# Kernel optimization log

Measured on AMD Instinct MI355X. Metric: run time of the kernel, lower is better.

## Reference

```python
import jax, jax.numpy as jnp
import numpy as np
import math

B, N, C = 4, 8192, 384
H = 6
D = C // H  # head_dim = 64


def setup_inputs() -> dict:
    key = jax.random.key(0)
    ks = jax.random.split(key, 9)
    s = 1.0 / math.sqrt(D)
    x = jax.random.normal(ks[0], (B, N, C), dtype=jnp.float32)
    Wq = jax.random.normal(ks[1], (H, D, D), dtype=jnp.float32) * s
    bq = jax.random.normal(ks[2], (H, D), dtype=jnp.float32) * 0.01
    Wk = jax.random.normal(ks[3], (H, D, D), dtype=jnp.float32) * s
    bk = jax.random.normal(ks[4], (H, D), dtype=jnp.float32) * 0.01
    Wv = jax.random.normal(ks[5], (H, D, D), dtype=jnp.float32) * s
    bv = jax.random.normal(ks[6], (H, D), dtype=jnp.float32) * 0.01
    Wp = jax.random.normal(ks[7], (C, C), dtype=jnp.float32) * (1.0 / math.sqrt(C))
    bp = jax.random.normal(ks[8], (C,), dtype=jnp.float32) * 0.01
    return {"x": x, "Wq": Wq, "bq": bq, "Wk": Wk, "bk": bk,
            "Wv": Wv, "bv": bv, "Wp": Wp, "bp": bp}


def reference(x, Wq, bq, Wk, bk, Wv, bv, Wp, bp):
    b, n, c = x.shape
    # [B, H, N, D]
    xh = x.reshape(b, n, H, D).transpose(0, 2, 1, 3)
    # Batched per-head projections (replaces the Python loop of per-head Linears)
    q = jnp.einsum('bhnd,hde->bhne', xh, Wq) + bq[:, None, :]
    k = jnp.einsum('bhnd,hde->bhne', xh, Wk) + bk[:, None, :]
    v = jnp.einsum('bhnd,hde->bhne', xh, Wv) + bv[:, None, :]
    q = jax.nn.softmax(q, axis=-1)          # over feature dim
    k = jax.nn.softmax(k, axis=-2)          # over sequence dim
    v = v * (1.0 / math.sqrt(D))
    kv = jnp.einsum('bhnd,bhne->bhde', k, v)   # [B,H,D,D] context
    out = jnp.einsum('bhnd,bhde->bhne', q, kv) # [B,H,N,D]
    out = out.transpose(0, 2, 1, 3).reshape(b, n, c)
    return out @ Wp.T + bp
```

## Files before the change

### kernel.cpp

```cpp
#include <hip/hip_runtime.h>
#include <hip/hip_bf16.h>


#define B 4
#define N 8192
#define C 384
#define H 6
#define D 64
#define BH (B * H)
#define BN (B * N)

typedef __attribute__((ext_vector_type(8))) short short8;
typedef __attribute__((ext_vector_type(4))) float f32x4;

__device__ inline unsigned short f2bf(float f) {
    unsigned int u = __float_as_uint(f);
    unsigned int r = (u + 0x7fff + ((u >> 16) & 1)) >> 16;
    return (unsigned short)r;
}

__device__ inline unsigned int cvt2bf(float a, float b) {
    unsigned int r;
    asm("v_cvt_pk_bf16_f32 %0, %1, %2" : "=v"(r) : "v"(a), "v"(b));
    return r;
}

__global__ void wprep(const float* __restrict__ Wq, const float* __restrict__ Wk,
                      const float* __restrict__ Wv, unsigned short* __restrict__ Wt,
                      float* __restrict__ kvraw)
{
    __shared__ float tmp[64][65];
    const int m = blockIdx.x / H;
    const int h = blockIdx.x % H;
    const float* in = (m == 0 ? Wq : m == 1 ? Wk : Wv) + h * 64 * 64;
    const int t = threadIdx.x;
    for (int d = 0; d < 64; ++d) tmp[d][t] = in[d * 64 + t];
    __syncthreads();
    const size_t base = ((size_t)(m * H + h)) * 64 * 64;
    for (int e = 0; e < 64; ++e)
        Wt[base + e * 64 + t] = f2bf(tmp[t][e]);

    const int gid = blockIdx.x * 64 + t;
    const float4 z = {0.f, 0.f, 0.f, 0.f};
    for (int i = gid; i < 24960; i += 1152)
        *(float4*)&kvraw[i * 4] = z;
}

__global__ __launch_bounds__(256, 3) void proj_kernel(
    const float* __restrict__ x, const unsigned short* __restrict__ Wt,
    const float* __restrict__ bq, const float* __restrict__ bk,
    const float* __restrict__ bv,
    unsigned short* __restrict__ qout,
    float* __restrict__ kvraw, float* __restrict__ Sg)
{
    __shared__ __align__(16) char smem[34816];
    unsigned short* W_s = (unsigned short*)smem;
    unsigned short* qbuf = (unsigned short*)(smem + 24576);
    float* kvred = (float*)smem;
    float* sred  = (float*)(smem + 33792);

    const int blk = blockIdx.x;
    const int nb  = blk & 31;
    const int bh  = blk >> 5;
    const int b   = bh / H;
    const int h   = bh % H;
    const int n0  = nb * 256;
    const int t   = threadIdx.x;
    const int lane = t & 63;
    const int w   = t >> 6;
    const int lq  = lane & 15;
    const int qd  = lane >> 4;

    {
        const size_t hb = (size_t)h * 4096;
        for (int id = t; id < 512; id += 256) {
            int e = id >> 3, c = id & 7;
            int dc = ((c ^ (e & 7)) * 8);
            #pragma unroll
            for (int m = 0; m < 3; ++m)
                *(uint4*)&W_s[m * 4096 + e * 64 + dc] =
                    *(const uint4*)(Wt + (size_t)m * H * 4096 + hb + e * 64 + c * 8);
        }
    }

    float bqv[4], bkv[4], bvv[4];
    #pragma unroll
    for (int j = 0; j < 4; ++j) {
        int col = j * 16 + lq;
        bqv[j] = bq[h * D + col];
        bkv[j] = bk[h * D + col];
        bvv[j] = bv[h * D + col];
    }

    unsigned short* qw = qbuf + w * 1152;

    __syncthreads();

    f32x4 kvacc[4][4] = {};
    float sacc[4] = {};

    for (int sub = 0; sub < 4; ++sub) {
        const int ns = n0 + sub * 64;

        const float* ap = x + (size_t)(b * N + ns + w * 16 + lq) * C + h * D + qd * 8;
        short8 af[2];
        {
            float av[16];
            *(float4*)&av[0]  = *(const float4*)ap;
            *(float4*)&av[4]  = *(const float4*)(ap + 4);
            *(float4*)&av[8]  = *(const float4*)(ap + 32);
            *(float4*)&av[12] = *(const float4*)(ap + 36);
            unsigned int* afu = (unsigned int*)af;
            #pragma unroll
            for (int p = 0; p < 8; ++p)
                afu[p] = cvt2bf(av[2 * p], av[2 * p + 1]);
        }

        {
            f32x4 acc[4] = {};
            #pragma unroll
            for (int ck = 0; ck < 2; ++ck)
                #pragma unroll
                for (int j = 0; j < 4; ++j) {
                    const int pc = ((ck * 4 + qd) ^ (lq & 7)) * 8;
                    short8 bw = *(const short8*)&W_s[(j * 16 + lq) * 64 + pc];
                    acc[j] = __builtin_amdgcn_mfma_f32_16x16x32_bf16(af[ck], bw, acc[j], 0, 0, 0);
                }
            #pragma unroll
            for (int r = 0; r < 4; ++r) {
                float e0 = __expf(acc[0][r] + bqv[0]);
                float e1 = __expf(acc[1][r] + bqv[1]);
                float e2 = __expf(acc[2][r] + bqv[2]);
                float e3 = __expf(acc[3][r] + bqv[3]);
                float s = (e0 + e1) + (e2 + e3);
                #pragma unroll
                for (int msk = 1; msk < 16; msk <<= 1) s += __shfl_xor(s, msk);
                float inv = __builtin_amdgcn_rcpf(s);
                unsigned int p01 = cvt2bf(e0 * inv, e1 * inv);
                unsigned int p23 = cvt2bf(e2 * inv, e3 * inv);
                const int row = qd * 4 + r;
                qw[row * 72 + 0 * 16 + lq] = (unsigned short)p01;
                qw[row * 72 + 1 * 16 + lq] = (unsigned short)(p01 >> 16);
                qw[row * 72 + 2 * 16 + lq] = (unsigned short)p23;
                qw[row * 72 + 3 * 16 + lq] = (unsigned short)(p23 >> 16);
            }
            const size_t gbase = (size_t)bh * N + ns + w * 16;
            #pragma unroll
            for (int rep = 0; rep < 2; ++rep) {
                int flat = rep * 64 + lane;
                int row = flat >> 3, c8 = flat & 7;
                *(uint4*)&qout[(gbase + row) * 64 + c8 * 8] =
                    *(uint4*)&qw[row * 72 + c8 * 8];
            }
        }
        __builtin_amdgcn_sched_barrier(0);

        short8 kfrag[4];
        {
            f32x4 acc[4] = {};
            #pragma unroll
            for (int ck = 0; ck < 2; ++ck)
                #pragma unroll
                for (int j = 0; j < 4; ++j) {
                    const int pc = ((ck * 4 + qd) ^ (lq & 7)) * 8;
                    short8 bw = *(const short8*)&W_s[4096 + (j * 16 + lq) * 64 + pc];
                    acc[j] = __builtin_amdgcn_mfma_f32_16x16x32_bf16(af[ck], bw, acc[j], 0, 0, 0);
                }
            #pragma unroll
            for (int j = 0; j < 4; ++j) {
                float e0 = __expf(acc[j][0] + bkv[j]);
                float e1 = __expf(acc[j][1] + bkv[j]);
                float e2 = __expf(acc[j][2] + bkv[j]);
                float e3 = __expf(acc[j][3] + bkv[j]);
                float cs = (e0 + e1) + (e2 + e3);
                cs += __shfl_xor(cs, 16);
                cs += __shfl_xor(cs, 32);
                sacc[j] += cs;
                unsigned int* kf = (unsigned int*)&kfrag[j];
                kf[0] = cvt2bf(e0, e1);
                kf[1] = cvt2bf(e2, e3);
                kf[2] = 0;
                kf[3] = 0;
            }
        }
        __builtin_amdgcn_sched_barrier(0);

        {
            f32x4 acc[4] = {};
            #pragma unroll
            for (int ck = 0; ck < 2; ++ck)
                #pragma unroll
                for (int j = 0; j < 4; ++j) {
                    const int pc = ((ck * 4 + qd) ^ (lq & 7)) * 8;
                    short8 bw = *(const short8*)&W_s[2 * 4096 + (j * 16 + lq) * 64 + pc];
                    acc[j] = __builtin_amdgcn_mfma_f32_16x16x32_bf16(af[ck], bw, acc[j], 0, 0, 0);
                }
            short8 vfrag[4];
            #pragma unroll
            for (int j = 0; j < 4; ++j) {
                float v0 = (acc[j][0] + bvv[j]) * 0.125f;
                float v1 = (acc[j][1] + bvv[j]) * 0.125f;
                float v2 = (acc[j][2] + bvv[j]) * 0.125f;
                float v3 = (acc[j][3] + bvv[j]) * 0.125f;
                unsigned int* vf = (unsigned int*)&vfrag[j];
                vf[0] = cvt2bf(v0, v1);
                vf[1] = cvt2bf(v2, v3);
                vf[2] = 0;
                vf[3] = 0;
            }
            #pragma unroll
            for (int i = 0; i < 4; ++i)
                #pragma unroll
                for (int j = 0; j < 4; ++j)
                    kvacc[i][j] = __builtin_amdgcn_mfma_f32_16x16x32_bf16(
                        kfrag[i], vfrag[j], kvacc[i][j], 0, 0, 0);
        }
        __builtin_amdgcn_sched_barrier(0);
    }

    __syncthreads();

    #pragma unroll
    for (int half = 0; half < 2; ++half) {
        #pragma unroll
        for (int i2 = 0; i2 < 2; ++i2) {
            const int ii = half * 2 + i2;
            #pragma unroll
            for (int j = 0; j < 4; ++j)
                #pragma unroll
                for (int r = 0; r < 4; ++r)
                    kvred[w * 2112 + (i2 * 16 + qd * 4 + r) * 66 + j * 16 + lq] =
                        kvacc[ii][j][r];
        }
        if (half == 0 && qd == 0) {
            #pragma unroll
            for (int j = 0; j < 4; ++j) sred[w * 64 + j * 16 + lq] = sacc[j];
        }
        __syncthreads();
        for (int idx = t; idx < 2048; idx += 256) {
            int dl = idx >> 6, e = idx & 63;
            float s = kvred[dl * 66 + e] + kvred[2112 + dl * 66 + e]
                    + kvred[2 * 2112 + dl * 66 + e] + kvred[3 * 2112 + dl * 66 + e];
            atomicAdd(&kvraw[bh * 4096 + (half * 32 + dl) * 64 + e], s);
        }
        if (half == 1 && t < 64) {
            float s = sred[t] + sred[64 + t] + sred[128 + t] + sred[192 + t];
            atomicAdd(&Sg[bh * 64 + t], s);
        }
        if (half == 0) __syncthreads();
    }
}

__global__ __launch_bounds__(256) void kw_kernel(
    const float* __restrict__ kvraw, const float* __restrict__ Sg,
    const float* __restrict__ Wp, unsigned short* __restrict__ KWT)
{
    __shared__ float kv_s[64 * 68];
    __shared__ float w_s[64 * 68];
    __shared__ float rS_s[64];
    const int bh = blockIdx.x / (C / 64);
    const int ct = blockIdx.x % (C / 64);
    const int b = bh / H, h = bh % H;
    const int c0 = ct * 64;
    const int t = threadIdx.x, dg = t >> 4, cg = t & 15;

    if (t < 64) rS_s[t] = 1.f / Sg[bh * 64 + t];
    __syncthreads();

    for (int i = t; i < 4096; i += 256) {
        int row = i >> 6, e = i & 63;
        kv_s[e * 68 + row] = kvraw[bh * (D * D) + row * 64 + e] * rS_s[row];
        w_s[e * 68 + row]  = Wp[(size_t)(c0 + row) * C + h * 64 + e];
    }
    __syncthreads();

    float acc[4][4] = {};
    for (int e = 0; e < 64; ++e) {
        float4 a = *(float4*)&kv_s[e * 68 + dg * 4];
        float4 w = *(float4*)&w_s[e * 68 + cg * 4];
        const float a4[4] = {a.x, a.y, a.z, a.w};
        const float w4[4] = {w.x, w.y, w.z, w.w};
        #pragma unroll
        for (int i = 0; i < 4; ++i)
            #pragma unroll
            for (int j = 0; j < 4; ++j) acc[i][j] += a4[i] * w4[j];
    }
    #pragma unroll
    for (int i = 0; i < 4; ++i)
        #pragma unroll
        for (int j = 0; j < 4; ++j) {
            int d = dg * 4 + i, c = c0 + cg * 4 + j;
            KWT[((size_t)b * C + c) * (H * D) + h * 64 + d] = f2bf(acc[i][j]);
        }
}

__global__ __launch_bounds__(256) void out_gemm(
    const unsigned short* __restrict__ q, const unsigned short* __restrict__ KWT,
    const float* __restrict__ bp, float* __restrict__ out)
{
    __shared__ __align__(16) unsigned short A_s[128 * 72];
    __shared__ __align__(16) unsigned short B_s[128 * 72];

    const int bid = blockIdx.x;
    const int grp = bid / 24;
    const int rem = bid % 24;
    const int ct  = rem >> 3;
    const int mt  = grp * 8 + (rem & 7);
    const int m0 = mt * 128, c0 = ct * 128;
    const int b  = m0 >> 13;
    const int n0 = m0 & (N - 1);
    const int t  = threadIdx.x;
    const int lane = t & 63;
    const int w  = t >> 6;
    const int wm = w >> 1, wn = w & 1;
    const int lq = lane & 15;
    const int qd = lane >> 4;

    f32x4 acc[4][4] = {};

    for (int h = 0; h < H; ++h) {
        if (h) __syncthreads();
        const unsigned short* qb = q + (size_t)(b * H + h) * N * D + (size_t)n0 * D;
        const unsigned short* kb = KWT + ((size_t)b * C + c0) * (H * D) + h * 64;
        #pragma unroll
        for (int it = 0; it < 4; ++it) {
            int id = it * 256 + t;
            int r = id >> 3, c8 = id & 7;
            *(uint4*)&A_s[r * 72 + c8 * 8] = *(const uint4*)(qb + r * 64 + c8 * 8);
            *(uint4*)&B_s[r * 72 + c8 * 8] = *(const uint4*)(kb + (size_t)r * (H * D) + c8 * 8);
        }
        __syncthreads();

        #pragma unroll
        for (int kk = 0; kk < 64; kk += 32) {
            short8 af[4], bf[4];
            #pragma unroll
            for (int i = 0; i < 4; ++i)
                af[i] = *(short8*)&A_s[(wm * 64 + i * 16 + lq) * 72 + kk + qd * 8];
            #pragma unroll
            for (int j = 0; j < 4; ++j)
                bf[j] = *(short8*)&B_s[(wn * 64 + j * 16 + lq) * 72 + kk + qd * 8];
            #pragma unroll
            for (int i = 0; i < 4; ++i)
                #pragma unroll
                for (int j = 0; j < 4; ++j)
                    acc[i][j] = __builtin_amdgcn_mfma_f32_16x16x32_bf16(
                        af[i], bf[j], acc[i][j], 0, 0, 0);
        }
    }

    float bpv[4];
    #pragma unroll
    for (int j = 0; j < 4; ++j) bpv[j] = bp[c0 + wn * 64 + j * 16 + lq];

    #pragma unroll
    for (int i = 0; i < 4; ++i) {
        #pragma unroll
        for (int r = 0; r < 4; ++r) {
            size_t row = (size_t)m0 + wm * 64 + i * 16 + qd * 4 + r;
            float* orow = out + row * C + c0 + wn * 64;
            #pragma unroll
            for (int j = 0; j < 4; ++j)
                orow[j * 16 + lq] = acc[i][j][r] + bpv[j];
        }
    }
}

extern "C" void kernel_launch(void* const* d_in, const int* in_sizes, int n_in,
                              void* d_out, int out_size, void* d_ws, size_t ws_size,
                              hipStream_t stream)
{
    const float* x  = (const float*)d_in[0];
    const float* Wq = (const float*)d_in[1];
    const float* bq = (const float*)d_in[2];
    const float* Wk = (const float*)d_in[3];
    const float* bk = (const float*)d_in[4];
    const float* Wv = (const float*)d_in[5];
    const float* bv = (const float*)d_in[6];
    const float* Wp = (const float*)d_in[7];
    const float* bp = (const float*)d_in[8];
    float* out = (float*)d_out;

    const size_t SZ = (size_t)B * H * N * D;
    float* ws   = (float*)d_ws;
    unsigned short* q = (unsigned short*)ws;
    float* kvraw = ws + SZ;
    float* Sg    = kvraw + (size_t)BH * D * D;
    unsigned short* KWT = (unsigned short*)(Sg + BH * 64);
    unsigned short* Wt  = KWT + (size_t)B * C * (H * D);

    wprep<<<3 * H, 64, 0, stream>>>(Wq, Wk, Wv, Wt, kvraw);
    proj_kernel<<<BH * (N / 256), 256, 0, stream>>>(x, Wt, bq, bk, bv,
                                                    q, kvraw, Sg);
    kw_kernel<<<BH * (C / 64), 256, 0, stream>>>(kvraw, Sg, Wp, KWT);
    out_gemm<<<(BN / 128) * (C / 128), 256, 0, stream>>>(q, KWT, bp, out);
}
```

Before: 150.9 us.

## Double-buffer out_gemm LDS tiles with register prefetch across heads

The output GEMM now keeps two LDS buffers for the q and KWT tiles. It loads the next head's tiles into registers while MFMAs run on the current buffer, then writes them to the other buffer with a single barrier per head. This is meant to hide global-load latency behind compute. The change doubles LDS use in out_gemm and adds registers, which may lower occupancy. Separately, proj_kernel's launch bound drops from 3 to 2 blocks per SM, allowing more registers per thread.

```diff
diff --git a/kernel.cpp b/kernel.cpp
--- a/kernel.cpp
+++ b/kernel.cpp
@@ -46,7 +46,7 @@
         *(float4*)&kvraw[i * 4] = z;
 }
 
-__global__ __launch_bounds__(256, 3) void proj_kernel(
+__global__ __launch_bounds__(256, 2) void proj_kernel(
     const float* __restrict__ x, const unsigned short* __restrict__ Wt,
     const float* __restrict__ bq, const float* __restrict__ bk,
     const float* __restrict__ bv,
@@ -298,8 +298,8 @@
     const unsigned short* __restrict__ q, const unsigned short* __restrict__ KWT,
     const float* __restrict__ bp, float* __restrict__ out)
 {
-    __shared__ __align__(16) unsigned short A_s[128 * 72];
-    __shared__ __align__(16) unsigned short B_s[128 * 72];
+    __shared__ __align__(16) unsigned short A_s[2][128 * 72];
+    __shared__ __align__(16) unsigned short B_s[2][128 * 72];
 
     const int bid = blockIdx.x;
     const int grp = bid / 24;
@@ -315,37 +315,61 @@
     const int wm = w >> 1, wn = w & 1;
     const int lq = lane & 15;
     const int qd = lane >> 4;
+    const int sr = t >> 3, sc8 = t & 7;
+
+    const unsigned short* qbase = q + (size_t)(b * H) * N * D + (size_t)n0 * D;
+    const unsigned short* kbase = KWT + ((size_t)b * C + c0) * (H * D);
 
     f32x4 acc[4][4] = {};
+    uint4 pa[4], pb[4];
+
+    #pragma unroll
+    for (int it = 0; it < 4; ++it) {
+        int r = sr + it * 32;
+        *(uint4*)&A_s[0][r * 72 + sc8 * 8] = *(const uint4*)(qbase + r * 64 + sc8 * 8);
+        *(uint4*)&B_s[0][r * 72 + sc8 * 8] = *(const uint4*)(kbase + (size_t)r * (H * D) + sc8 * 8);
+    }
+    __syncthreads();
 
     for (int h = 0; h < H; ++h) {
-        if (h) __syncthreads();
-        const unsigned short* qb = q + (size_t)(b * H + h) * N * D + (size_t)n0 * D;
-        const unsigned short* kb = KWT + ((size_t)b * C + c0) * (H * D) + h * 64;
-        #pragma unroll
-        for (int it = 0; it < 4; ++it) {
-            int id = it * 256 + t;
-            int r = id >> 3, c8 = id & 7;
-            *(uint4*)&A_s[r * 72 + c8 * 8] = *(const uint4*)(qb + r * 64 + c8 * 8);
-            *(uint4*)&B_s[r * 72 + c8 * 8] = *(const uint4*)(kb + (size_t)r * (H * D) + c8 * 8);
-        }
-        __syncthreads();
+        const int cur = h & 1;
+
+        if (h + 1 < H) {
+            const unsigned short* qb = qbase + (size_t)(h + 1) * N * D;
+            const unsigned short* kb = kbase + (h + 1) * 64;
+            #pragma unroll
+            for (int it = 0; it < 4; ++it) {
+                int r = sr + it * 32;
+                pa[it] = *(const uint4*)(qb + r * 64 + sc8 * 8);
+                pb[it] = *(const uint4*)(kb + (size_t)r * (H * D) + sc8 * 8);
+            }
+        }
 
         #pragma unroll
         for (int kk = 0; kk < 64; kk += 32) {
             short8 af[4], bf[4];
             #pragma unroll
             for (int i = 0; i < 4; ++i)
-                af[i] = *(short8*)&A_s[(wm * 64 + i * 16 + lq) * 72 + kk + qd * 8];
+                af[i] = *(short8*)&A_s[cur][(wm * 64 + i * 16 + lq) * 72 + kk + qd * 8];
             #pragma unroll
             for (int j = 0; j < 4; ++j)
-                bf[j] = *(short8*)&B_s[(wn * 64 + j * 16 + lq) * 72 + kk + qd * 8];
+                bf[j] = *(short8*)&B_s[cur][(wn * 64 + j * 16 + lq) * 72 + kk + qd * 8];
             #pragma unroll
             for (int i = 0; i < 4; ++i)
                 #pragma unroll
                 for (int j = 0; j < 4; ++j)
                     acc[i][j] = __builtin_amdgcn_mfma_f32_16x16x32_bf16(
                         af[i], bf[j], acc[i][j], 0, 0, 0);
+        }
+
+        if (h + 1 < H) {
+            #pragma unroll
+            for (int it = 0; it < 4; ++it) {
+                int r = sr + it * 32;
+                *(uint4*)&A_s[cur ^ 1][r * 72 + sc8 * 8] = pa[it];
+                *(uint4*)&B_s[cur ^ 1][r * 72 + sc8 * 8] = pb[it];
+            }
+            __syncthreads();
         }
     }
 
```

Measured after the change: 168.8 us. +11.8%, slower.
